# Performance work log

Measured on AMD Instinct MI355X. Metric: run time of the kernel, lower is better.

The kernel has to match this reference:

```python
import jax, jax.numpy as jnp
import numpy as np

LECUN_A = 1.7159
LECUN_B = 0.666


def lecun_tanh(x):
    return LECUN_A * jnp.tanh(LECUN_B * x)


def setup_inputs() -> dict:
    key = jax.random.key(0)
    ks = jax.random.split(key, 12)
    B, T, I, H, U = 128, 1024, 256, 512, 1024
    s_in = 1.0 / np.sqrt(I + H)
    s_u = 1.0 / np.sqrt(U)
    return {
        "input": jax.random.normal(ks[0], (B, T, I), jnp.float32),
        "hx": jax.random.normal(ks[1], (B, T, H), jnp.float32),
        "ts": jax.random.uniform(ks[2], (B, T), jnp.float32),
        "W0": jax.random.normal(ks[3], (I + H, U), jnp.float32) * s_in,
        "b0": jnp.zeros((U,), jnp.float32),
        "W1": jax.random.normal(ks[4], (U, U), jnp.float32) * s_u,
        "b1": jnp.zeros((U,), jnp.float32),
        "W_ff1": jax.random.normal(ks[5], (U, H), jnp.float32) * s_u,
        "b_ff1": jnp.zeros((H,), jnp.float32),
        "W_ff2": jax.random.normal(ks[6], (U, H), jnp.float32) * s_u,
        "b_ff2": jnp.zeros((H,), jnp.float32),
        "W_ta": jax.random.normal(ks[7], (U, H), jnp.float32) * s_u,
        "b_ta": jnp.zeros((H,), jnp.float32),
        "W_tb": jax.random.normal(ks[8], (U, H), jnp.float32) * s_u,
        "b_tb": jnp.zeros((H,), jnp.float32),
    }


def reference(input, hx, ts, W0, b0, W1, b1, W_ff1, b_ff1, W_ff2, b_ff2,
              W_ta, b_ta, W_tb, b_tb):
    # x: [B, T, I+H]
    x = jnp.concatenate([input, hx], axis=2)
    # backbone: Linear -> LeCun -> Linear -> LeCun
    x = lecun_tanh(jnp.einsum("btc,cu->btu", x, W0) + b0)
    x = lecun_tanh(jnp.einsum("btu,uv->btv", x, W1) + b1)
    # four parallel heads sharing x: [B, T, H] each
    ff1 = jnp.tanh(jnp.einsum("btu,uh->bth", x, W_ff1) + b_ff1)
    ff2 = jnp.tanh(jnp.einsum("btu,uh->bth", x, W_ff2) + b_ff2)
    t_a = jnp.einsum("btu,uh->bth", x, W_ta) + b_ta
    t_b = jnp.einsum("btu,uh->bth", x, W_tb) + b_tb
    # time-gated interpolation
    t_interp = jax.nn.sigmoid(t_a * ts[:, :, None] + t_b)
    new_hidden = ff1 * (1.0 - t_interp) + t_interp * ff2
    return new_hidden
```

## Files before the change

### kernel.cpp

```cpp
#include <hip/hip_runtime.h>
#include <hip/hip_bf16.h>


typedef unsigned short u16;
typedef __bf16 bf16x8_t __attribute__((ext_vector_type(8)));
typedef float f32x4_t __attribute__((ext_vector_type(4)));
typedef u16 u16x8_t __attribute__((ext_vector_type(8)));

#define M_TOTAL 131072

__device__ __forceinline__ u16 f2bf(float f) {
  union { float f; unsigned u; } v; v.f = f;
  unsigned r = v.u + 0x7FFFu + ((v.u >> 16) & 1u);
  return (u16)(r >> 16);
}

__device__ __forceinline__ float fast_tanh(float x) {
  x = fminf(15.f, fmaxf(-15.f, x));
  float e = __expf(2.f * x);
  return (e - 1.f) * __builtin_amdgcn_rcpf(e + 1.f);
}

__device__ __forceinline__ float fast_sigmoid(float x) {
  return __builtin_amdgcn_rcpf(1.f + __expf(-x));
}

__device__ __forceinline__ void gload_lds16(const void* g, void* l) {
  __builtin_amdgcn_global_load_lds(
      (const __attribute__((address_space(1))) unsigned int*)g,
      (__attribute__((address_space(3))) unsigned int*)l,
      16, 0, 0);
}


__global__ void prep_x(const float* __restrict__ inp, const float* __restrict__ hx,
                       u16* __restrict__ X) {
  const int total = M_TOTAL * 96;
  int stride = gridDim.x * blockDim.x;
  for (int v = blockIdx.x * blockDim.x + threadIdx.x; v < total; v += stride) {
    int m = v / 96; int c = v - m * 96;
    const float* src = (c < 32) ? (inp + (size_t)m * 256 + (c << 3))
                                : (hx + (size_t)m * 512 + ((size_t)(c - 32) << 3));
    f32x4_t a = *(const f32x4_t*)src;
    f32x4_t b = *(const f32x4_t*)(src + 4);
    u16x8_t o;
    o[0]=f2bf(a[0]); o[1]=f2bf(a[1]); o[2]=f2bf(a[2]); o[3]=f2bf(a[3]);
    o[4]=f2bf(b[0]); o[5]=f2bf(b[1]); o[6]=f2bf(b[2]); o[7]=f2bf(b[3]);
    *(u16x8_t*)(X + (size_t)m * 768 + (c << 3)) = o;
  }
}

__global__ void prep_wt(const float* __restrict__ W, u16* __restrict__ WT,
                        int K, int N, int head) {
  int id = blockIdx.x * blockDim.x + threadIdx.x;
  int k8s = K >> 3;
  int total = N * k8s;
  if (id >= total) return;
  int n = id / k8s;
  int k0 = (id - n * k8s) << 3;
  u16x8_t o;
#pragma unroll
  for (int i = 0; i < 8; ++i) o[i] = f2bf(W[(size_t)(k0 + i) * N + n]);
  int row = (head < 0) ? n : (((n >> 4) << 6) + head * 16 + (n & 15));
  *(u16x8_t*)(WT + (size_t)row * K + k0) = o;
}

__global__ void prep_bias(const float* __restrict__ b1, const float* __restrict__ b2,
                          const float* __restrict__ b3, const float* __restrict__ b4,
                          float* __restrict__ bi) {
  int h = blockIdx.x * blockDim.x + threadIdx.x;
  if (h < 512) {
    int base = ((h >> 4) << 6) + (h & 15);
    bi[base +  0] = b1[h];
    bi[base + 16] = b2[h];
    bi[base + 32] = b3[h];
    bi[base + 48] = b4[h];
  }
}


#define BARX()  do { __builtin_amdgcn_s_barrier(); __builtin_amdgcn_sched_barrier(0); } while(0)
#define LGKM0() do { asm volatile("s_waitcnt lgkmcnt(0)" ::: "memory"); __builtin_amdgcn_sched_barrier(0); } while(0)

template<int K, int NI, int EPI>
__global__ __launch_bounds__(512, 2)
void gemm256(const u16* __restrict__ A, const u16* __restrict__ BT,
             const float* __restrict__ bias, const float* __restrict__ ts,
             void* __restrict__ Cout)
{
  constexpr int NTn = NI / 256;
  constexpr int NITER = K / 128;
  constexpr int NWG = (M_TOTAL / 256) * NTn;
  __shared__ __align__(16) char smem[131072];

  const int bid0 = blockIdx.x;
  const int bid = (bid0 & 7) * (NWG >> 3) + (bid0 >> 3);
  const int mt = bid / NTn, nt = bid % NTn;
  const int tileM = mt * 256, tileN = nt * 256;

  const int tid = threadIdx.x;
  const int w = tid >> 6, l = tid & 63;
  const int wm = w >> 2, wn = w & 3;

  const int c0 = w * 2, c1 = w * 2 + 1;
  const int kkS0 = c0 >> 3, kkS1 = c1 >> 3;
  const int rS0 = (c0 & 7) * 16 + (l >> 2);
  const int rS1 = (c1 & 7) * 16 + (l >> 2);
  const int cbS = ((l & 3) << 4) ^ (((l >> 5) & 1) << 5);
  const int cA0 = (c0 & 7) * 1024, cA1 = (c1 & 7) * 1024;
  const u16* aSrc = A + (size_t)tileM * K + (cbS >> 1);
  const u16* bSrc = BT + (size_t)tileN * K + (cbS >> 1);

  const int colRs = ((l >> 4) * 16) ^ (((l >> 3) & 1) << 5);
  const int aRowB = (wm * 128 + (l & 15)) * 64;
  const int bRowB = 65536 + (wn * 64 + (l & 15)) * 64;

  const int colBase = tileN + wn * 64 + (l & 15);
  float bv[4];
  bv[0] = bias[colBase];      bv[1] = bias[colBase + 16];
  bv[2] = bias[colBase + 32]; bv[3] = bias[colBase + 48];

  f32x4_t acc[8][4];
#pragma unroll
  for (int i = 0; i < 8; ++i)
#pragma unroll
    for (int j = 0; j < 4; ++j) acc[i][j] = f32x4_t{0.f, 0.f, 0.f, 0.f};

  bf16x8_t af[4][2], b01[2][2], b23[2][2];

#define STAGE_A(d, h, t) do { \
    gload_lds16(aSrc + (size_t)((h)*128 + rS0) * K + (t)*64 + kkS0*32, \
                smem + (d)*32768 + kkS0*16384 + (h)*8192 + cA0); \
    gload_lds16(aSrc + (size_t)((h)*128 + rS1) * K + (t)*64 + kkS1*32, \
                smem + (d)*32768 + kkS1*16384 + (h)*8192 + cA1); } while(0)

#define STAGE_B(d, h, t) do { \
    gload_lds16(bSrc + (size_t)((h)*128 + rS0) * K + (t)*64 + kkS0*32, \
                smem + 65536 + (d)*32768 + kkS0*16384 + (h)*8192 + cA0); \
    gload_lds16(bSrc + (size_t)((h)*128 + rS1) * K + (t)*64 + kkS1*32, \
                smem + 65536 + (d)*32768 + kkS1*16384 + (h)*8192 + cA1); } while(0)

#define READ_A(d, mb) do { \
    _Pragma("unroll") for (int mm_ = 0; mm_ < 4; ++mm_) { \
      af[mm_][0] = *(const bf16x8_t*)(smem + (d)*32768 +         aRowB + ((mb)+mm_)*1024 + colRs); \
      af[mm_][1] = *(const bf16x8_t*)(smem + (d)*32768 + 16384 + aRowB + ((mb)+mm_)*1024 + colRs); } } while(0)

#define READ_B(d, breg, nb) do { \
    _Pragma("unroll") for (int nn_ = 0; nn_ < 2; ++nn_) { \
      breg[nn_][0] = *(const bf16x8_t*)(smem + (d)*32768 +         bRowB + ((nb)+nn_)*1024 + colRs); \
      breg[nn_][1] = *(const bf16x8_t*)(smem + (d)*32768 + 16384 + bRowB + ((nb)+nn_)*1024 + colRs); } } while(0)

#define MFMAQ(mb, nb, breg) do { \
    __builtin_amdgcn_s_setprio(1); \
    _Pragma("unroll") for (int kk_ = 0; kk_ < 2; ++kk_) \
      _Pragma("unroll") for (int mm_ = 0; mm_ < 4; ++mm_) \
        _Pragma("unroll") for (int nn_ = 0; nn_ < 2; ++nn_) \
          acc[(mb)+mm_][(nb)+nn_] = __builtin_amdgcn_mfma_f32_16x16x32_bf16( \
              af[mm_][kk_], breg[nn_][kk_], acc[(mb)+mm_][(nb)+nn_], 0, 0, 0); \
    __builtin_amdgcn_s_setprio(0); \
  } while(0)

  STAGE_A(0, 0, 0); STAGE_A(0, 1, 0);
  STAGE_B(0, 0, 0); STAGE_B(0, 1, 0);
  STAGE_B(1, 0, 1); STAGE_B(1, 1, 1);
  asm volatile("s_waitcnt vmcnt(4)" ::: "memory");
  BARX();

#pragma unroll 1
  for (int i = 0; i < NITER; ++i) {
    const int t1 = 2*i + 1, t2 = 2*i + 2, t3 = 2*i + 3;
    const bool more = (i + 1 < NITER);
    READ_A(0, 0); READ_B(0, b01, 0);
    STAGE_A(1, 0, t1);
    BARX(); LGKM0(); MFMAQ(0, 0, b01); BARX();
    READ_B(0, b23, 2);
    STAGE_A(1, 1, t1);
    BARX(); LGKM0(); MFMAQ(0, 2, b23); BARX();
    READ_A(0, 4);
    if (more) STAGE_B(0, 0, t2);
    BARX(); LGKM0(); MFMAQ(4, 0, b01); BARX();
    if (more) STAGE_B(0, 1, t2);
    BARX(); MFMAQ(4, 2, b23);
    if (more) { asm volatile("s_waitcnt vmcnt(4)" ::: "memory"); }
    else      { asm volatile("s_waitcnt vmcnt(0)" ::: "memory"); }
    BARX();
    READ_A(1, 0); READ_B(1, b01, 0);
    if (more) STAGE_A(0, 0, t2);
    BARX(); LGKM0(); MFMAQ(0, 0, b01); BARX();
    READ_B(1, b23, 2);
    if (more) STAGE_A(0, 1, t2);
    BARX(); LGKM0(); MFMAQ(0, 2, b23); BARX();
    READ_A(1, 4);
    if (more) STAGE_B(1, 0, t3);
    BARX(); LGKM0(); MFMAQ(4, 0, b01); BARX();
    if (more) STAGE_B(1, 1, t3);
    BARX(); MFMAQ(4, 2, b23);
    asm volatile("s_waitcnt vmcnt(4)" ::: "memory");
    BARX();
  }

  if constexpr (EPI == 0) {
    u16* C = (u16*)Cout;
#pragma unroll
    for (int m = 0; m < 8; ++m)
#pragma unroll
      for (int nn = 0; nn < 4; ++nn)
#pragma unroll
        for (int j = 0; j < 4; ++j) {
          const int row = tileM + wm*128 + m*16 + ((l >> 4) << 2) + j;
          float v = acc[m][nn][j] + bv[nn];
          float t = 1.7159f * fast_tanh(0.666f * v);
          C[(size_t)row * NI + colBase + nn*16] = f2bf(t);
        }
  } else {
    if (tid < 256) ((float*)smem)[tid] = ts[tileM + tid];
    __syncthreads();
    const int hg = ((tileN + wn*64) >> 6) * 16 + (l & 15);
    float* out = (float*)Cout;
#pragma unroll
    for (int m = 0; m < 8; ++m)
#pragma unroll
      for (int j = 0; j < 4; ++j) {
        const int rl = wm*128 + m*16 + ((l >> 4) << 2) + j;
        const float tsv = ((const float*)smem)[rl];
        float ff1 = fast_tanh(acc[m][0][j] + bv[0]);
        float ff2 = fast_tanh(acc[m][1][j] + bv[1]);
        float s = fast_sigmoid((acc[m][2][j] + bv[2]) * tsv + (acc[m][3][j] + bv[3]));
        out[(size_t)(tileM + rl) * 512 + hg] = ff1 + s * (ff2 - ff1);
      }
  }
#undef STAGE_A
#undef STAGE_B
#undef READ_A
#undef READ_B
#undef MFMAQ
}


extern "C" void kernel_launch(void* const* d_in, const int* in_sizes, int n_in,
                              void* d_out, int out_size, void* d_ws, size_t ws_size,
                              hipStream_t stream) {
  const float* input = (const float*)d_in[0];
  const float* hx    = (const float*)d_in[1];
  const float* ts    = (const float*)d_in[2];
  const float* W0    = (const float*)d_in[3];
  const float* b0    = (const float*)d_in[4];
  const float* W1    = (const float*)d_in[5];
  const float* b1    = (const float*)d_in[6];
  const float* Wff1  = (const float*)d_in[7];
  const float* bff1  = (const float*)d_in[8];
  const float* Wff2  = (const float*)d_in[9];
  const float* bff2  = (const float*)d_in[10];
  const float* Wta   = (const float*)d_in[11];
  const float* bta   = (const float*)d_in[12];
  const float* Wtb   = (const float*)d_in[13];
  const float* btb   = (const float*)d_in[14];

  const size_t WS_NEEDED = 544743424ull;
  if (ws_size < WS_NEEDED) return;
  char* ws = (char*)d_ws;
  u16* Xcat = (u16*)(ws);
  u16* X2   = (u16*)(ws);
  u16* X1   = (u16*)(ws + 268435456ull);
  u16* W0T  = (u16*)(ws + 536870912ull);
  u16* W1T  = (u16*)(ws + 538443776ull);
  u16* WhT  = (u16*)(ws + 540540928ull);
  float* biasi = (float*)(ws + 544735232ull);

  prep_x<<<2048, 256, 0, stream>>>(input, hx, Xcat);
  prep_wt<<<(1024 * 96 + 255) / 256, 256, 0, stream>>>(W0, W0T, 768, 1024, -1);
  prep_wt<<<(1024 * 128 + 255) / 256, 256, 0, stream>>>(W1, W1T, 1024, 1024, -1);
  prep_wt<<<(512 * 128 + 255) / 256, 256, 0, stream>>>(Wff1, WhT, 1024, 512, 0);
  prep_wt<<<(512 * 128 + 255) / 256, 256, 0, stream>>>(Wff2, WhT, 1024, 512, 1);
  prep_wt<<<(512 * 128 + 255) / 256, 256, 0, stream>>>(Wta,  WhT, 1024, 512, 2);
  prep_wt<<<(512 * 128 + 255) / 256, 256, 0, stream>>>(Wtb,  WhT, 1024, 512, 3);
  prep_bias<<<2, 256, 0, stream>>>(bff1, bff2, bta, btb, biasi);

  gemm256<768, 1024, 0><<<2048, 512, 0, stream>>>(Xcat, W0T, b0, nullptr, X1);
  gemm256<1024, 1024, 0><<<2048, 512, 0, stream>>>(X1, W1T, b1, nullptr, X2);
  gemm256<1024, 2048, 1><<<4096, 512, 0, stream>>>(X2, WhT, biasi, ts, d_out);
}
```

Measured before the change: 1.213 ms.

## Make GEMMs persistent over multiple tiles and prefetch next tile across boundaries

Each GEMM launches 256 workgroups, and each one walks a contiguous run of tiles (8 or 16). The last k-iteration of a tile stages the first k-slices of the next tile, so global loads overlap the epilogue and no pipeline drains between tiles. The seven weight and bias prep launches are also merged into a single prep kernel. In exchange, the blockIdx swizzle for L2 locality is dropped, each tile's ts values are read straight from global memory, and 256 workgroups at two per CU may not fill every CU on the chip.

After: 1.398 ms. +15.3%, slower.

```diff
diff --git a/kernel.cpp b/kernel.cpp
--- a/kernel.cpp
+++ b/kernel.cpp
@@ -50,39 +50,49 @@
   }
 }
 
-__global__ void prep_wt(const float* __restrict__ W, u16* __restrict__ WT,
-                        int K, int N, int head) {
+__global__ void prep_w(const float* __restrict__ W0, const float* __restrict__ W1,
+                       const float* __restrict__ Wf1, const float* __restrict__ Wf2,
+                       const float* __restrict__ Wta, const float* __restrict__ Wtb,
+                       const float* __restrict__ bf1, const float* __restrict__ bf2,
+                       const float* __restrict__ bta, const float* __restrict__ btb,
+                       u16* __restrict__ W0T, u16* __restrict__ W1T,
+                       u16* __restrict__ WhT, float* __restrict__ biasi) {
   int id = blockIdx.x * blockDim.x + threadIdx.x;
-  int k8s = K >> 3;
-  int total = N * k8s;
-  if (id >= total) return;
-  int n = id / k8s;
-  int k0 = (id - n * k8s) << 3;
   u16x8_t o;
-#pragma unroll
-  for (int i = 0; i < 8; ++i) o[i] = f2bf(W[(size_t)(k0 + i) * N + n]);
-  int row = (head < 0) ? n : (((n >> 4) << 6) + head * 16 + (n & 15));
-  *(u16x8_t*)(WT + (size_t)row * K + k0) = o;
-}
-
-__global__ void prep_bias(const float* __restrict__ b1, const float* __restrict__ b2,
-                          const float* __restrict__ b3, const float* __restrict__ b4,
-                          float* __restrict__ bi) {
-  int h = blockIdx.x * blockDim.x + threadIdx.x;
-  if (h < 512) {
+  if (id < 98304) {
+    int n = id / 96, k0 = (id - n * 96) << 3;
+#pragma unroll
+    for (int i = 0; i < 8; ++i) o[i] = f2bf(W0[(size_t)(k0 + i) * 1024 + n]);
+    *(u16x8_t*)(W0T + (size_t)n * 768 + k0) = o;
+  } else if (id < 229376) {
+    int id2 = id - 98304; int n = id2 >> 7, k0 = (id2 & 127) << 3;
+#pragma unroll
+    for (int i = 0; i < 8; ++i) o[i] = f2bf(W1[(size_t)(k0 + i) * 1024 + n]);
+    *(u16x8_t*)(W1T + (size_t)n * 1024 + k0) = o;
+  } else if (id < 491520) {
+    int id3 = id - 229376; int head = id3 >> 16; int id4 = id3 & 65535;
+    int n = id4 >> 7, k0 = (id4 & 127) << 3;
+    const float* W = (head == 0) ? Wf1 : (head == 1) ? Wf2 : (head == 2) ? Wta : Wtb;
+#pragma unroll
+    for (int i = 0; i < 8; ++i) o[i] = f2bf(W[(size_t)(k0 + i) * 512 + n]);
+    int row = ((n >> 4) << 6) + head * 16 + (n & 15);
+    *(u16x8_t*)(WhT + (size_t)row * 1024 + k0) = o;
+  } else if (id < 492032) {
+    int h = id - 491520;
     int base = ((h >> 4) << 6) + (h & 15);
-    bi[base +  0] = b1[h];
-    bi[base + 16] = b2[h];
-    bi[base + 32] = b3[h];
-    bi[base + 48] = b4[h];
+    biasi[base +  0] = bf1[h];
+    biasi[base + 16] = bf2[h];
+    biasi[base + 32] = bta[h];
+    biasi[base + 48] = btb[h];
   }
 }
 
 
 #define BARX()  do { __builtin_amdgcn_s_barrier(); __builtin_amdgcn_sched_barrier(0); } while(0)
 #define LGKM0() do { asm volatile("s_waitcnt lgkmcnt(0)" ::: "memory"); __builtin_amdgcn_sched_barrier(0); } while(0)
-
-template<int K, int NI, int EPI>
+#define VMC4()  do { asm volatile("s_waitcnt vmcnt(4)" ::: "memory"); } while(0)
+
+template<int K, int NI, int EPI, int TPB>
 __global__ __launch_bounds__(512, 2)
 void gemm256(const u16* __restrict__ A, const u16* __restrict__ BT,
              const float* __restrict__ bias, const float* __restrict__ ts,
@@ -90,13 +100,7 @@
 {
   constexpr int NTn = NI / 256;
   constexpr int NITER = K / 128;
-  constexpr int NWG = (M_TOTAL / 256) * NTn;
   __shared__ __align__(16) char smem[131072];
-
-  const int bid0 = blockIdx.x;
-  const int bid = (bid0 & 7) * (NWG >> 3) + (bid0 >> 3);
-  const int mt = bid / NTn, nt = bid % NTn;
-  const int tileM = mt * 256, tileN = nt * 256;
 
   const int tid = threadIdx.x;
   const int w = tid >> 6, l = tid & 63;
@@ -108,36 +112,25 @@
   const int rS1 = (c1 & 7) * 16 + (l >> 2);
   const int cbS = ((l & 3) << 4) ^ (((l >> 5) & 1) << 5);
   const int cA0 = (c0 & 7) * 1024, cA1 = (c1 & 7) * 1024;
-  const u16* aSrc = A + (size_t)tileM * K + (cbS >> 1);
-  const u16* bSrc = BT + (size_t)tileN * K + (cbS >> 1);
+  const int laneK = cbS >> 1;
 
   const int colRs = ((l >> 4) * 16) ^ (((l >> 3) & 1) << 5);
   const int aRowB = (wm * 128 + (l & 15)) * 64;
   const int bRowB = 65536 + (wn * 64 + (l & 15)) * 64;
 
-  const int colBase = tileN + wn * 64 + (l & 15);
-  float bv[4];
-  bv[0] = bias[colBase];      bv[1] = bias[colBase + 16];
-  bv[2] = bias[colBase + 32]; bv[3] = bias[colBase + 48];
-
   f32x4_t acc[8][4];
-#pragma unroll
-  for (int i = 0; i < 8; ++i)
-#pragma unroll
-    for (int j = 0; j < 4; ++j) acc[i][j] = f32x4_t{0.f, 0.f, 0.f, 0.f};
-
   bf16x8_t af[4][2], b01[2][2], b23[2][2];
 
-#define STAGE_A(d, h, t) do { \
-    gload_lds16(aSrc + (size_t)((h)*128 + rS0) * K + (t)*64 + kkS0*32, \
+#define STAGE_A(d, h, SRC, t) do { \
+    gload_lds16((SRC) + (size_t)((h)*128 + rS0) * K + (t)*64 + kkS0*32, \
                 smem + (d)*32768 + kkS0*16384 + (h)*8192 + cA0); \
-    gload_lds16(aSrc + (size_t)((h)*128 + rS1) * K + (t)*64 + kkS1*32, \
+    gload_lds16((SRC) + (size_t)((h)*128 + rS1) * K + (t)*64 + kkS1*32, \
                 smem + (d)*32768 + kkS1*16384 + (h)*8192 + cA1); } while(0)
 
-#define STAGE_B(d, h, t) do { \
-    gload_lds16(bSrc + (size_t)((h)*128 + rS0) * K + (t)*64 + kkS0*32, \
+#define STAGE_B(d, h, SRC, t) do { \
+    gload_lds16((SRC) + (size_t)((h)*128 + rS0) * K + (t)*64 + kkS0*32, \
                 smem + 65536 + (d)*32768 + kkS0*16384 + (h)*8192 + cA0); \
-    gload_lds16(bSrc + (size_t)((h)*128 + rS1) * K + (t)*64 + kkS1*32, \
+    gload_lds16((SRC) + (size_t)((h)*128 + rS1) * K + (t)*64 + kkS1*32, \
                 smem + 65536 + (d)*32768 + kkS1*16384 + (h)*8192 + cA1); } while(0)
 
 #define READ_A(d, mb) do { \
@@ -160,80 +153,107 @@
     __builtin_amdgcn_s_setprio(0); \
   } while(0)
 
-  STAGE_A(0, 0, 0); STAGE_A(0, 1, 0);
-  STAGE_B(0, 0, 0); STAGE_B(0, 1, 0);
-  STAGE_B(1, 0, 1); STAGE_B(1, 1, 1);
-  asm volatile("s_waitcnt vmcnt(4)" ::: "memory");
-  BARX();
+#define ITER(ii, A2, B2, T2, T3) do { \
+    READ_A(0, 0); READ_B(0, b01, 0); \
+    STAGE_A(1, 0, aCur, 2*(ii)+1); \
+    BARX(); LGKM0(); MFMAQ(0, 0, b01); BARX(); \
+    READ_B(0, b23, 2); \
+    STAGE_A(1, 1, aCur, 2*(ii)+1); \
+    BARX(); LGKM0(); MFMAQ(0, 2, b23); BARX(); \
+    READ_A(0, 4); \
+    STAGE_B(0, 0, B2, T2); \
+    BARX(); LGKM0(); MFMAQ(4, 0, b01); BARX(); \
+    STAGE_B(0, 1, B2, T2); \
+    BARX(); MFMAQ(4, 2, b23); \
+    VMC4(); BARX(); \
+    READ_A(1, 0); READ_B(1, b01, 0); \
+    STAGE_A(0, 0, A2, T2); \
+    BARX(); LGKM0(); MFMAQ(0, 0, b01); BARX(); \
+    READ_B(1, b23, 2); \
+    STAGE_A(0, 1, A2, T2); \
+    BARX(); LGKM0(); MFMAQ(0, 2, b23); BARX(); \
+    READ_A(1, 4); \
+    STAGE_B(1, 0, B2, T3); \
+    BARX(); LGKM0(); MFMAQ(4, 0, b01); BARX(); \
+    STAGE_B(1, 1, B2, T3); \
+    BARX(); MFMAQ(4, 2, b23); \
+    VMC4(); BARX(); \
+  } while(0)
+
+  const int tile0 = blockIdx.x * TPB;
+
+  {
+    const int mt0 = tile0 / NTn, nt0 = tile0 % NTn;
+    const u16* a0 = A + (size_t)(mt0 * 256) * K + laneK;
+    const u16* b0 = BT + (size_t)(nt0 * 256) * K + laneK;
+    STAGE_A(0, 0, a0, 0); STAGE_A(0, 1, a0, 0);
+    STAGE_B(0, 0, b0, 0); STAGE_B(0, 1, b0, 0);
+    STAGE_B(1, 0, b0, 1); STAGE_B(1, 1, b0, 1);
+    VMC4(); BARX();
+  }
 
 #pragma unroll 1
-  for (int i = 0; i < NITER; ++i) {
-    const int t1 = 2*i + 1, t2 = 2*i + 2, t3 = 2*i + 3;
-    const bool more = (i + 1 < NITER);
-    READ_A(0, 0); READ_B(0, b01, 0);
-    STAGE_A(1, 0, t1);
-    BARX(); LGKM0(); MFMAQ(0, 0, b01); BARX();
-    READ_B(0, b23, 2);
-    STAGE_A(1, 1, t1);
-    BARX(); LGKM0(); MFMAQ(0, 2, b23); BARX();
-    READ_A(0, 4);
-    if (more) STAGE_B(0, 0, t2);
-    BARX(); LGKM0(); MFMAQ(4, 0, b01); BARX();
-    if (more) STAGE_B(0, 1, t2);
-    BARX(); MFMAQ(4, 2, b23);
-    if (more) { asm volatile("s_waitcnt vmcnt(4)" ::: "memory"); }
-    else      { asm volatile("s_waitcnt vmcnt(0)" ::: "memory"); }
-    BARX();
-    READ_A(1, 0); READ_B(1, b01, 0);
-    if (more) STAGE_A(0, 0, t2);
-    BARX(); LGKM0(); MFMAQ(0, 0, b01); BARX();
-    READ_B(1, b23, 2);
-    if (more) STAGE_A(0, 1, t2);
-    BARX(); LGKM0(); MFMAQ(0, 2, b23); BARX();
-    READ_A(1, 4);
-    if (more) STAGE_B(1, 0, t3);
-    BARX(); LGKM0(); MFMAQ(4, 0, b01); BARX();
-    if (more) STAGE_B(1, 1, t3);
-    BARX(); MFMAQ(4, 2, b23);
-    asm volatile("s_waitcnt vmcnt(4)" ::: "memory");
-    BARX();
-  }
-
-  if constexpr (EPI == 0) {
-    u16* C = (u16*)Cout;
-#pragma unroll
-    for (int m = 0; m < 8; ++m)
-#pragma unroll
-      for (int nn = 0; nn < 4; ++nn)
+  for (int tt = 0; tt < TPB; ++tt) {
+    const int tcur = tile0 + tt;
+    const int tnxt = (tt + 1 < TPB) ? tcur + 1 : tcur;
+    const int tileM = (tcur / NTn) * 256, tileN = (tcur % NTn) * 256;
+    const u16* aCur = A + (size_t)tileM * K + laneK;
+    const u16* bCur = BT + (size_t)tileN * K + laneK;
+    const u16* aNxt = A + (size_t)((tnxt / NTn) * 256) * K + laneK;
+    const u16* bNxt = BT + (size_t)((tnxt % NTn) * 256) * K + laneK;
+
+    const int colBase = tileN + wn * 64 + (l & 15);
+    float bv[4];
+    bv[0] = bias[colBase];      bv[1] = bias[colBase + 16];
+    bv[2] = bias[colBase + 32]; bv[3] = bias[colBase + 48];
+
+#pragma unroll
+    for (int i = 0; i < 8; ++i)
+#pragma unroll
+      for (int j = 0; j < 4; ++j) acc[i][j] = f32x4_t{0.f, 0.f, 0.f, 0.f};
+
+#pragma unroll 1
+    for (int i = 0; i < NITER - 1; ++i) ITER(i, aCur, bCur, 2 * i + 2, 2 * i + 3);
+    ITER(NITER - 1, aNxt, bNxt, 0, 1);
+
+    if constexpr (EPI == 0) {
+      u16* C = (u16*)Cout;
+      const int rowB = tileM + wm * 128 + ((l >> 4) << 2);
+#pragma unroll
+      for (int m = 0; m < 8; ++m)
+#pragma unroll
+        for (int nn = 0; nn < 4; ++nn)
+#pragma unroll
+          for (int j = 0; j < 4; ++j) {
+            float v = acc[m][nn][j] + bv[nn];
+            float t = 1.7159f * fast_tanh(0.666f * v);
+            C[(size_t)(rowB + m * 16 + j) * NI + colBase + nn * 16] = f2bf(t);
+          }
+    } else {
+      const int hg = ((tileN + wn * 64) >> 6) * 16 + (l & 15);
+      float* out = (float*)Cout;
+#pragma unroll
+      for (int m = 0; m < 8; ++m)
 #pragma unroll
         for (int j = 0; j < 4; ++j) {
-          const int row = tileM + wm*128 + m*16 + ((l >> 4) << 2) + j;
-          float v = acc[m][nn][j] + bv[nn];
-          float t = 1.7159f * fast_tanh(0.666f * v);
-          C[(size_t)row * NI + colBase + nn*16] = f2bf(t);
+          const int rl = wm * 128 + m * 16 + ((l >> 4) << 2) + j;
+          const float tsv = ts[tileM + rl];
+          float ff1 = fast_tanh(acc[m][0][j] + bv[0]);
+          float ff2 = fast_tanh(acc[m][1][j] + bv[1]);
+          float s = fast_sigmoid((acc[m][2][j] + bv[2]) * tsv + (acc[m][3][j] + bv[3]));
+          out[(size_t)(tileM + rl) * 512 + hg] = ff1 + s * (ff2 - ff1);
         }
-  } else {
-    if (tid < 256) ((float*)smem)[tid] = ts[tileM + tid];
-    __syncthreads();
-    const int hg = ((tileN + wn*64) >> 6) * 16 + (l & 15);
-    float* out = (float*)Cout;
-#pragma unroll
-    for (int m = 0; m < 8; ++m)
-#pragma unroll
-      for (int j = 0; j < 4; ++j) {
-        const int rl = wm*128 + m*16 + ((l >> 4) << 2) + j;
-        const float tsv = ((const float*)smem)[rl];
-        float ff1 = fast_tanh(acc[m][0][j] + bv[0]);
-        float ff2 = fast_tanh(acc[m][1][j] + bv[1]);
-        float s = fast_sigmoid((acc[m][2][j] + bv[2]) * tsv + (acc[m][3][j] + bv[3]));
-        out[(size_t)(tileM + rl) * 512 + hg] = ff1 + s * (ff2 - ff1);
-      }
-  }
+    }
+  }
+
+  asm volatile("s_waitcnt vmcnt(0)" ::: "memory");
+
 #undef STAGE_A
 #undef STAGE_B
 #undef READ_A
 #undef READ_B
 #undef MFMAQ
+#undef ITER
 }
 
 
@@ -268,15 +288,10 @@
   float* biasi = (float*)(ws + 544735232ull);
 
   prep_x<<<2048, 256, 0, stream>>>(input, hx, Xcat);
-  prep_wt<<<(1024 * 96 + 255) / 256, 256, 0, stream>>>(W0, W0T, 768, 1024, -1);
-  prep_wt<<<(1024 * 128 + 255) / 256, 256, 0, stream>>>(W1, W1T, 1024, 1024, -1);
-  prep_wt<<<(512 * 128 + 255) / 256, 256, 0, stream>>>(Wff1, WhT, 1024, 512, 0);
-  prep_wt<<<(512 * 128 + 255) / 256, 256, 0, stream>>>(Wff2, WhT, 1024, 512, 1);
-  prep_wt<<<(512 * 128 + 255) / 256, 256, 0, stream>>>(Wta,  WhT, 1024, 512, 2);
-  prep_wt<<<(512 * 128 + 255) / 256, 256, 0, stream>>>(Wtb,  WhT, 1024, 512, 3);
-  prep_bias<<<2, 256, 0, stream>>>(bff1, bff2, bta, btb, biasi);
-
-  gemm256<768, 1024, 0><<<2048, 512, 0, stream>>>(Xcat, W0T, b0, nullptr, X1);
-  gemm256<1024, 1024, 0><<<2048, 512, 0, stream>>>(X1, W1T, b1, nullptr, X2);
-  gemm256<1024, 2048, 1><<<4096, 512, 0, stream>>>(X2, WhT, biasi, ts, d_out);
-}
+  prep_w<<<1922, 256, 0, stream>>>(W0, W1, Wff1, Wff2, Wta, Wtb,
+                                   bff1, bff2, bta, btb, W0T, W1T, WhT, biasi);
+
+  gemm256<768, 1024, 0, 8><<<256, 512, 0, stream>>>(Xcat, W0T, b0, nullptr, X1);
+  gemm256<1024, 1024, 0, 8><<<256, 512, 0, stream>>>(X1, W1T, b1, nullptr, X2);
+  gemm256<1024, 2048, 1, 16><<<256, 512, 0, stream>>>(X2, WhT, biasi, ts, d_out);
+}
```

## Switch GEMMs to 32x32x16 MFMA tiles and merge weight prep kernels

Applied to the files above, without the earlier changes.

Replaces the 16x16x32 bf16 MFMA inner tiles with 32x32x16 MFMAs. This halves the number of MFMA instructions and changes the LDS fragment read pattern and accumulator layout. The epilogue is rewritten for the new layout and uses lane shuffles to pair the ff1/ff2 and ta/tb heads, reading ts directly from global memory instead of staging it in LDS. The six weight-transpose launches and the bias launch are folded into one prep kernel to cut launch overhead. Risks are LDS bank conflicts in the new read pattern, and half the lanes doing redundant transcendental work in the head epilogue.

Measured after the change: 1.451 ms. 1.2x slower.

```diff
diff --git a/kernel.cpp b/kernel.cpp
--- a/kernel.cpp
+++ b/kernel.cpp
@@ -5,6 +5,7 @@
 typedef unsigned short u16;
 typedef __bf16 bf16x8_t __attribute__((ext_vector_type(8)));
 typedef float f32x4_t __attribute__((ext_vector_type(4)));
+typedef float f32x16_t __attribute__((ext_vector_type(16)));
 typedef u16 u16x8_t __attribute__((ext_vector_type(8)));
 
 #define M_TOTAL 131072
@@ -50,31 +51,40 @@
   }
 }
 
-__global__ void prep_wt(const float* __restrict__ W, u16* __restrict__ WT,
-                        int K, int N, int head) {
+__global__ void prep_w(const float* __restrict__ W0, const float* __restrict__ W1,
+                       const float* __restrict__ Wf1, const float* __restrict__ Wf2,
+                       const float* __restrict__ Wta, const float* __restrict__ Wtb,
+                       const float* __restrict__ bf1, const float* __restrict__ bf2,
+                       const float* __restrict__ bta, const float* __restrict__ btb,
+                       u16* __restrict__ W0T, u16* __restrict__ W1T,
+                       u16* __restrict__ WhT, float* __restrict__ biasi) {
   int id = blockIdx.x * blockDim.x + threadIdx.x;
-  int k8s = K >> 3;
-  int total = N * k8s;
-  if (id >= total) return;
-  int n = id / k8s;
-  int k0 = (id - n * k8s) << 3;
   u16x8_t o;
-#pragma unroll
-  for (int i = 0; i < 8; ++i) o[i] = f2bf(W[(size_t)(k0 + i) * N + n]);
-  int row = (head < 0) ? n : (((n >> 4) << 6) + head * 16 + (n & 15));
-  *(u16x8_t*)(WT + (size_t)row * K + k0) = o;
-}
-
-__global__ void prep_bias(const float* __restrict__ b1, const float* __restrict__ b2,
-                          const float* __restrict__ b3, const float* __restrict__ b4,
-                          float* __restrict__ bi) {
-  int h = blockIdx.x * blockDim.x + threadIdx.x;
-  if (h < 512) {
+  if (id < 98304) {
+    int n = id / 96, k0 = (id - n * 96) << 3;
+#pragma unroll
+    for (int i = 0; i < 8; ++i) o[i] = f2bf(W0[(size_t)(k0 + i) * 1024 + n]);
+    *(u16x8_t*)(W0T + (size_t)n * 768 + k0) = o;
+  } else if (id < 229376) {
+    int id2 = id - 98304; int n = id2 >> 7, k0 = (id2 & 127) << 3;
+#pragma unroll
+    for (int i = 0; i < 8; ++i) o[i] = f2bf(W1[(size_t)(k0 + i) * 1024 + n]);
+    *(u16x8_t*)(W1T + (size_t)n * 1024 + k0) = o;
+  } else if (id < 491520) {
+    int id3 = id - 229376; int head = id3 >> 16; int id4 = id3 & 65535;
+    int n = id4 >> 7, k0 = (id4 & 127) << 3;
+    const float* W = (head == 0) ? Wf1 : (head == 1) ? Wf2 : (head == 2) ? Wta : Wtb;
+#pragma unroll
+    for (int i = 0; i < 8; ++i) o[i] = f2bf(W[(size_t)(k0 + i) * 512 + n]);
+    int row = ((n >> 4) << 6) + head * 16 + (n & 15);
+    *(u16x8_t*)(WhT + (size_t)row * 1024 + k0) = o;
+  } else if (id < 492032) {
+    int h = id - 491520;
     int base = ((h >> 4) << 6) + (h & 15);
-    bi[base +  0] = b1[h];
-    bi[base + 16] = b2[h];
-    bi[base + 32] = b3[h];
-    bi[base + 48] = b4[h];
+    biasi[base +  0] = bf1[h];
+    biasi[base + 16] = bf2[h];
+    biasi[base + 32] = bta[h];
+    biasi[base + 48] = btb[h];
   }
 }
 
@@ -84,9 +94,9 @@
 
 template<int K, int NI, int EPI>
 __global__ __launch_bounds__(512, 2)
-void gemm256(const u16* __restrict__ A, const u16* __restrict__ BT,
-             const float* __restrict__ bias, const float* __restrict__ ts,
-             void* __restrict__ Cout)
+void gemm32(const u16* __restrict__ A, const u16* __restrict__ BT,
+            const float* __restrict__ bias, const float* __restrict__ ts,
+            void* __restrict__ Cout)
 {
   constexpr int NTn = NI / 256;
   constexpr int NITER = K / 128;
@@ -111,22 +121,21 @@
   const u16* aSrc = A + (size_t)tileM * K + (cbS >> 1);
   const u16* bSrc = BT + (size_t)tileN * K + (cbS >> 1);
 
-  const int colRs = ((l >> 4) * 16) ^ (((l >> 3) & 1) << 5);
-  const int aRowB = (wm * 128 + (l & 15)) * 64;
-  const int bRowB = 65536 + (wn * 64 + (l & 15)) * 64;
-
-  const int colBase = tileN + wn * 64 + (l & 15);
-  float bv[4];
-  bv[0] = bias[colBase];      bv[1] = bias[colBase + 16];
-  bv[2] = bias[colBase + 32]; bv[3] = bias[colBase + 48];
-
-  f32x4_t acc[8][4];
-#pragma unroll
-  for (int i = 0; i < 8; ++i)
-#pragma unroll
-    for (int j = 0; j < 4; ++j) acc[i][j] = f32x4_t{0.f, 0.f, 0.f, 0.f};
-
-  bf16x8_t af[4][2], b01[2][2], b23[2][2];
+  const int xb = (l & 8) << 2;
+  const int rc0 = ((l >> 5) << 4) + xb;
+  const int rc1 = ((l >> 5) << 4) + (32 ^ xb);
+  const char* aBase = (const char*)smem + (wm * 128 + (l & 31)) * 64;
+  const char* bBase = (const char*)smem + 65536 + (wn * 64 + (l & 31)) * 64;
+
+  f32x16_t acc[4][2];
+#pragma unroll
+  for (int i = 0; i < 4; ++i)
+#pragma unroll
+    for (int j = 0; j < 2; ++j)
+#pragma unroll
+      for (int e = 0; e < 16; ++e) acc[i][j][e] = 0.f;
+
+  bf16x8_t aq[2][2][2], b0q[2][2], b1q[2][2];
 
 #define STAGE_A(d, h, t) do { \
     gload_lds16(aSrc + (size_t)((h)*128 + rS0) * K + (t)*64 + kkS0*32, \
@@ -140,23 +149,27 @@
     gload_lds16(bSrc + (size_t)((h)*128 + rS1) * K + (t)*64 + kkS1*32, \
                 smem + 65536 + (d)*32768 + kkS1*16384 + (h)*8192 + cA1); } while(0)
 
-#define READ_A(d, mb) do { \
-    _Pragma("unroll") for (int mm_ = 0; mm_ < 4; ++mm_) { \
-      af[mm_][0] = *(const bf16x8_t*)(smem + (d)*32768 +         aRowB + ((mb)+mm_)*1024 + colRs); \
-      af[mm_][1] = *(const bf16x8_t*)(smem + (d)*32768 + 16384 + aRowB + ((mb)+mm_)*1024 + colRs); } } while(0)
-
-#define READ_B(d, breg, nb) do { \
-    _Pragma("unroll") for (int nn_ = 0; nn_ < 2; ++nn_) { \
-      breg[nn_][0] = *(const bf16x8_t*)(smem + (d)*32768 +         bRowB + ((nb)+nn_)*1024 + colRs); \
-      breg[nn_][1] = *(const bf16x8_t*)(smem + (d)*32768 + 16384 + bRowB + ((nb)+nn_)*1024 + colRs); } } while(0)
-
-#define MFMAQ(mb, nb, breg) do { \
+#define READ_A(d, mp) do { \
+    _Pragma("unroll") for (int s_ = 0; s_ < 2; ++s_) { \
+      aq[0][s_][0] = *(const bf16x8_t*)(aBase + (d)*32768 + s_*16384 + ((mp)*2+0)*2048 + rc0); \
+      aq[0][s_][1] = *(const bf16x8_t*)(aBase + (d)*32768 + s_*16384 + ((mp)*2+0)*2048 + rc1); \
+      aq[1][s_][0] = *(const bf16x8_t*)(aBase + (d)*32768 + s_*16384 + ((mp)*2+1)*2048 + rc0); \
+      aq[1][s_][1] = *(const bf16x8_t*)(aBase + (d)*32768 + s_*16384 + ((mp)*2+1)*2048 + rc1); \
+    } } while(0)
+
+#define READ_B(d, BQ, nb) do { \
+    _Pragma("unroll") for (int s_ = 0; s_ < 2; ++s_) { \
+      BQ[s_][0] = *(const bf16x8_t*)(bBase + (d)*32768 + s_*16384 + (nb)*2048 + rc0); \
+      BQ[s_][1] = *(const bf16x8_t*)(bBase + (d)*32768 + s_*16384 + (nb)*2048 + rc1); \
+    } } while(0)
+
+#define MFMAQ(mp, nb, BQ) do { \
     __builtin_amdgcn_s_setprio(1); \
-    _Pragma("unroll") for (int kk_ = 0; kk_ < 2; ++kk_) \
-      _Pragma("unroll") for (int mm_ = 0; mm_ < 4; ++mm_) \
-        _Pragma("unroll") for (int nn_ = 0; nn_ < 2; ++nn_) \
-          acc[(mb)+mm_][(nb)+nn_] = __builtin_amdgcn_mfma_f32_16x16x32_bf16( \
-              af[mm_][kk_], breg[nn_][kk_], acc[(mb)+mm_][(nb)+nn_], 0, 0, 0); \
+    _Pragma("unroll") for (int s_ = 0; s_ < 2; ++s_) \
+      _Pragma("unroll") for (int kk_ = 0; kk_ < 2; ++kk_) \
+        _Pragma("unroll") for (int mL_ = 0; mL_ < 2; ++mL_) \
+          acc[(mp)*2+mL_][nb] = __builtin_amdgcn_mfma_f32_32x32x16_bf16( \
+              aq[mL_][s_][kk_], BQ[s_][kk_], acc[(mp)*2+mL_][nb], 0, 0, 0); \
     __builtin_amdgcn_s_setprio(0); \
   } while(0)
 
@@ -170,63 +183,74 @@
   for (int i = 0; i < NITER; ++i) {
     const int t1 = 2*i + 1, t2 = 2*i + 2, t3 = 2*i + 3;
     const bool more = (i + 1 < NITER);
-    READ_A(0, 0); READ_B(0, b01, 0);
+    READ_A(0, 0); READ_B(0, b0q, 0);
     STAGE_A(1, 0, t1);
-    BARX(); LGKM0(); MFMAQ(0, 0, b01); BARX();
-    READ_B(0, b23, 2);
+    BARX(); LGKM0(); MFMAQ(0, 0, b0q); BARX();
+    READ_B(0, b1q, 1);
     STAGE_A(1, 1, t1);
-    BARX(); LGKM0(); MFMAQ(0, 2, b23); BARX();
-    READ_A(0, 4);
+    BARX(); LGKM0(); MFMAQ(0, 1, b1q); BARX();
+    READ_A(0, 1);
     if (more) STAGE_B(0, 0, t2);
-    BARX(); LGKM0(); MFMAQ(4, 0, b01); BARX();
+    BARX(); LGKM0(); MFMAQ(1, 0, b0q); BARX();
     if (more) STAGE_B(0, 1, t2);
-    BARX(); MFMAQ(4, 2, b23);
+    BARX(); MFMAQ(1, 1, b1q);
     if (more) { asm volatile("s_waitcnt vmcnt(4)" ::: "memory"); }
     else      { asm volatile("s_waitcnt vmcnt(0)" ::: "memory"); }
     BARX();
-    READ_A(1, 0); READ_B(1, b01, 0);
+    READ_A(1, 0); READ_B(1, b0q, 0);
     if (more) STAGE_A(0, 0, t2);
-    BARX(); LGKM0(); MFMAQ(0, 0, b01); BARX();
-    READ_B(1, b23, 2);
+    BARX(); LGKM0(); MFMAQ(0, 0, b0q); BARX();
+    READ_B(1, b1q, 1);
     if (more) STAGE_A(0, 1, t2);
-    BARX(); LGKM0(); MFMAQ(0, 2, b23); BARX();
-    READ_A(1, 4);
+    BARX(); LGKM0(); MFMAQ(0, 1, b1q); BARX();
+    READ_A(1, 1);
     if (more) STAGE_B(1, 0, t3);
-    BARX(); LGKM0(); MFMAQ(4, 0, b01); BARX();
+    BARX(); LGKM0(); MFMAQ(1, 0, b0q); BARX();
     if (more) STAGE_B(1, 1, t3);
-    BARX(); MFMAQ(4, 2, b23);
+    BARX(); MFMAQ(1, 1, b1q);
     asm volatile("s_waitcnt vmcnt(4)" ::: "memory");
     BARX();
   }
 
+  const int colB = tileN + wn * 64 + (l & 31);
+  const int rBase = tileM + wm * 128 + ((l >> 5) << 2);
+
   if constexpr (EPI == 0) {
+    const float bv0 = bias[colB], bv1 = bias[colB + 32];
     u16* C = (u16*)Cout;
 #pragma unroll
-    for (int m = 0; m < 8; ++m)
-#pragma unroll
-      for (int nn = 0; nn < 4; ++nn)
-#pragma unroll
-        for (int j = 0; j < 4; ++j) {
-          const int row = tileM + wm*128 + m*16 + ((l >> 4) << 2) + j;
-          float v = acc[m][nn][j] + bv[nn];
-          float t = 1.7159f * fast_tanh(0.666f * v);
-          C[(size_t)row * NI + colBase + nn*16] = f2bf(t);
-        }
+    for (int mb = 0; mb < 4; ++mb)
+#pragma unroll
+      for (int r = 0; r < 16; ++r) {
+        const int row = rBase + mb * 32 + (r & 3) + ((r >> 2) << 3);
+        float v0 = acc[mb][0][r] + bv0;
+        float v1 = acc[mb][1][r] + bv1;
+        C[(size_t)row * NI + colB]      = f2bf(1.7159f * fast_tanh(0.666f * v0));
+        C[(size_t)row * NI + colB + 32] = f2bf(1.7159f * fast_tanh(0.666f * v1));
+      }
   } else {
-    if (tid < 256) ((float*)smem)[tid] = ts[tileM + tid];
-    __syncthreads();
-    const int hg = ((tileN + wn*64) >> 6) * 16 + (l & 15);
+    const float bv0 = bias[colB], bv1 = bias[colB + 32];
+    const int hg = ((tileN >> 6) + wn) * 16 + (l & 15);
+    const bool low = ((l & 16) == 0);
     float* out = (float*)Cout;
 #pragma unroll
-    for (int m = 0; m < 8; ++m)
-#pragma unroll
-      for (int j = 0; j < 4; ++j) {
-        const int rl = wm*128 + m*16 + ((l >> 4) << 2) + j;
-        const float tsv = ((const float*)smem)[rl];
-        float ff1 = fast_tanh(acc[m][0][j] + bv[0]);
-        float ff2 = fast_tanh(acc[m][1][j] + bv[1]);
-        float s = fast_sigmoid((acc[m][2][j] + bv[2]) * tsv + (acc[m][3][j] + bv[3]));
-        out[(size_t)(tileM + rl) * 512 + hg] = ff1 + s * (ff2 - ff1);
+    for (int mb = 0; mb < 4; ++mb)
+#pragma unroll
+      for (int r = 0; r < 16; ++r) {
+        float a0 = acc[mb][0][r] + bv0;
+        float a1 = acc[mb][1][r] + bv1;
+        float e0 = __shfl_xor(a0, 16);
+        float e1 = __shfl_xor(a1, 16);
+        float ff1r = low ? a0 : e0;
+        float ff2r = low ? e0 : a0;
+        float tar  = low ? a1 : e1;
+        float tbr  = low ? e1 : a1;
+        const int row = rBase + mb * 32 + (r & 3) + ((r >> 2) << 3);
+        const float tsv = ts[row];
+        float s = fast_sigmoid(tar * tsv + tbr);
+        float f1 = fast_tanh(ff1r);
+        float f2 = fast_tanh(ff2r);
+        if (low) out[(size_t)row * 512 + hg] = f1 + s * (f2 - f1);
       }
   }
 #undef STAGE_A
@@ -268,15 +292,10 @@
   float* biasi = (float*)(ws + 544735232ull);
 
   prep_x<<<2048, 256, 0, stream>>>(input, hx, Xcat);
-  prep_wt<<<(1024 * 96 + 255) / 256, 256, 0, stream>>>(W0, W0T, 768, 1024, -1);
-  prep_wt<<<(1024 * 128 + 255) / 256, 256, 0, stream>>>(W1, W1T, 1024, 1024, -1);
-  prep_wt<<<(512 * 128 + 255) / 256, 256, 0, stream>>>(Wff1, WhT, 1024, 512, 0);
-  prep_wt<<<(512 * 128 + 255) / 256, 256, 0, stream>>>(Wff2, WhT, 1024, 512, 1);
-  prep_wt<<<(512 * 128 + 255) / 256, 256, 0, stream>>>(Wta,  WhT, 1024, 512, 2);
-  prep_wt<<<(512 * 128 + 255) / 256, 256, 0, stream>>>(Wtb,  WhT, 1024, 512, 3);
-  prep_bias<<<2, 256, 0, stream>>>(bff1, bff2, bta, btb, biasi);
-
-  gemm256<768, 1024, 0><<<2048, 512, 0, stream>>>(Xcat, W0T, b0, nullptr, X1);
-  gemm256<1024, 1024, 0><<<2048, 512, 0, stream>>>(X1, W1T, b1, nullptr, X2);
-  gemm256<1024, 2048, 1><<<4096, 512, 0, stream>>>(X2, WhT, biasi, ts, d_out);
-}
+  prep_w<<<1922, 256, 0, stream>>>(W0, W1, Wff1, Wff2, Wta, Wtb,
+                                   bff1, bff2, bta, btb, W0T, W1T, WhT, biasi);
+
+  gemm32<768, 1024, 0><<<2048, 512, 0, stream>>>(Xcat, W0T, b0, nullptr, X1);
+  gemm32<1024, 1024, 0><<<2048, 512, 0, stream>>>(X1, W1T, b1, nullptr, X2);
+  gemm32<1024, 2048, 1><<<4096, 512, 0, stream>>>(X2, WhT, biasi, ts, d_out);
+}
```
